# Optimization experiments

Hardware: AMD Instinct MI355X
Metric: run time of the kernel (lower is better)

The kernel has to match this reference:

```python
import jax, jax.numpy as jnp
import numpy as np

N, E, F, H, C = 50000, 800000, 128, 4, 32
SLOPE_ATT = 0.2   # PyG GATConv default negative_slope for attention logits
SLOPE_ACT = 0.01  # torch leaky_relu default between layers


def setup_inputs() -> dict:
    key = jax.random.key(0)
    ks = jax.random.split(key, 12)
    sc = 0.1
    return {
        "x": jax.random.normal(ks[0], (N, F), jnp.float32),
        "edge_index": jax.random.randint(ks[1], (2, E), 0, N, dtype=jnp.int32),
        "W1": jax.random.normal(ks[2], (F, H * C), jnp.float32) * sc,
        "a_src1": jax.random.normal(ks[3], (H, C), jnp.float32) * sc,
        "a_dst1": jax.random.normal(ks[4], (H, C), jnp.float32) * sc,
        "b1": jnp.zeros((H * C,), jnp.float32),
        "W2": jax.random.normal(ks[5], (H * C, H * C), jnp.float32) * sc,
        "a_src2": jax.random.normal(ks[6], (H, C), jnp.float32) * sc,
        "a_dst2": jax.random.normal(ks[7], (H, C), jnp.float32) * sc,
        "b2": jnp.zeros((H * C,), jnp.float32),
        "Wfc": jax.random.normal(ks[8], (H * C, 1), jnp.float32) * sc,
        "bfc": jnp.zeros((1,), jnp.float32),
    }


def gat_layer(x, src, dst, W, a_src, a_dst, bias):
    """PyG-style GATConv: per-head linear, edge attention with leaky_relu,
    segment-softmax over incoming edges of each dst node, scatter-add aggregate."""
    n = x.shape[0]
    h = (x @ W).reshape(n, H, C)                       # [N,H,C]
    att_s = jnp.einsum('nhc,hc->nh', h, a_src)         # per-node src logits
    att_d = jnp.einsum('nhc,hc->nh', h, a_dst)         # per-node dst logits
    e = jax.nn.leaky_relu(att_s[src] + att_d[dst], SLOPE_ATT)   # [Etot,H]
    m = jax.ops.segment_max(e, dst, num_segments=n)    # stable softmax per dst
    e = jnp.exp(e - m[dst])
    z = jax.ops.segment_sum(e, dst, num_segments=n)
    alpha = e / (z[dst] + 1e-16)                       # [Etot,H]
    out = jax.ops.segment_sum(alpha[:, :, None] * h[src], dst, num_segments=n)
    return out.reshape(n, H * C) + bias                # concat heads + bias


def reference(x, edge_index, W1, a_src1, a_dst1, b1, W2, a_src2, a_dst2, b2, Wfc, bfc):
    loops = jnp.arange(N, dtype=edge_index.dtype)      # PyG adds self-loops
    src = jnp.concatenate([edge_index[0], loops])
    dst = jnp.concatenate([edge_index[1], loops])
    h = jax.nn.leaky_relu(gat_layer(x, src, dst, W1, a_src1, a_dst1, b1), SLOPE_ACT)
    h = jax.nn.leaky_relu(gat_layer(h, src, dst, W2, a_src2, a_dst2, b2), SLOPE_ACT)
    return (h @ Wfc + bfc).squeeze(-1)                 # [N]
```

## Files before the change

### kernel.cpp

```cpp
#include <hip/hip_runtime.h>
#include <hip/hip_fp16.h>

#define FD 128

typedef __attribute__((ext_vector_type(8))) short bf16x8;
typedef __attribute__((ext_vector_type(4))) float f32x4;

__device__ __forceinline__ float lrelu(float x, float s){ return x > 0.f ? x : s*x; }

__device__ __forceinline__ unsigned short f2bf(float f){
  unsigned u = __builtin_bit_cast(unsigned, f);
  return (unsigned short)((u + 0x7FFFu + ((u >> 16) & 1u)) >> 16);
}
__device__ __forceinline__ float bf2f(unsigned short h){
  unsigned u = ((unsigned)h) << 16;
  return __builtin_bit_cast(float, u);
}


__global__ __launch_bounds__(256) void count_wprep_kernel(const int* __restrict__ dst,
    int* __restrict__ counts, int E, unsigned rscale, int nchunk, int nbc,
    const float* __restrict__ W1, const float* __restrict__ W2,
    const float* __restrict__ aS1, const float* __restrict__ aD1,
    const float* __restrict__ aS2, const float* __restrict__ aD2,
    unsigned short* __restrict__ WT1, unsigned short* __restrict__ WT2)
{
  int b = blockIdx.x;
  if (b < nbc){
    int xcd = b & 7, chunk = b >> 3;
    int nv = E >> 2;
    for (int v = chunk*256 + threadIdx.x; v < nv; v += nchunk*256){
      int4 d4 = ((const int4*)dst)[v];
      #pragma unroll
      for (int t = 0; t < 4; ++t){
        int d = (&d4.x)[t];
        unsigned r = (unsigned)(((unsigned long long)(unsigned)d * rscale) >> 32);
        if ((int)r == xcd) atomicAdd(&counts[d], 1);
      }
    }
    if (chunk == 0 && threadIdx.x < (E & 3)){
      int i = (E & ~3) + threadIdx.x;
      int d = dst[i];
      unsigned r = (unsigned)(((unsigned long long)(unsigned)d * rscale) >> 32);
      if ((int)r == xcd) atomicAdd(&counts[d], 1);
    }
    return;
  }
  int id = (b - nbc)*256 + threadIdx.x;
  if (id < 32768){
    const float* W = (id < 16384) ? W1 : W2;
    unsigned short* T = (id < 16384) ? WT1 : WT2;
    int idx = id & 16383;
    int k = idx >> 7, c = idx & 127;
    int w = ((c & 7) << 4) | (c >> 3);
    int si = w*128 + (k ^ ((w & 7) << 3));
    float v = W[idx];
    unsigned short h = f2bf(v);
    T[si] = h;
    T[18432 + si] = f2bf(v - bf2f(h));
  } else if (id < 34816){
    int id2 = id - 32768;
    int layer = id2 >> 10;
    int id3 = id2 & 1023;
    int k = id3 >> 3, cc = id3 & 7;
    const float* W  = layer ? W2 : W1;
    const float* av = (cc < 4) ? (layer ? aS2 : aS1) : (layer ? aD2 : aD1);
    unsigned short* T = layer ? WT2 : WT1;
    int h = cc & 3, base = h*32;
    float acc = 0.f;
    #pragma unroll 8
    for (int c = 0; c < 32; ++c) acc += W[k*FD + base + c] * av[base + c];
    int w = 128 + cc;
    int si = w*128 + (k ^ ((w & 7) << 3));
    unsigned short hh = f2bf(acc);
    T[si] = hh;
    T[18432 + si] = f2bf(acc - bf2f(hh));
  } else if (id < 36864){
    int id2 = id - 34816;
    int layer = id2 >> 10;
    int id3 = id2 & 1023;
    int w = 136 + (id3 >> 7), k = id3 & 127;
    unsigned short* T = layer ? WT2 : WT1;
    int si = w*128 + (k ^ ((w & 7) << 3));
    T[si] = 0;
    T[18432 + si] = 0;
  }
}

__global__ __launch_bounds__(512) void scan1_kernel(const int* __restrict__ counts,
    int* __restrict__ offsets, int* __restrict__ blocksum, int n){
  __shared__ int wsum[8];
  int tid = threadIdx.x, lane = tid & 63, wv = tid >> 6;
  int i = blockIdx.x*512 + tid;
  int v = (i < n) ? counts[i] + 1 : 0;
  int incl = v;
  #pragma unroll
  for (int off = 1; off < 64; off <<= 1){
    int t = __shfl_up(incl, off);
    if (lane >= off) incl += t;
  }
  if (lane == 63) wsum[wv] = incl;
  __syncthreads();
  if (wv == 0 && lane < 8){
    int s = wsum[lane];
    #pragma unroll
    for (int off = 1; off < 8; off <<= 1){
      int t = __shfl_up(s, off);
      if (lane >= off) s += t;
    }
    wsum[lane] = s;
  }
  __syncthreads();
  int woff = (wv > 0) ? wsum[wv-1] : 0;
  incl += woff;
  if (i < n) offsets[i] = incl;
  if (tid == 511) blocksum[blockIdx.x] = incl;
}

__global__ __launch_bounds__(512) void scan3_kernel(const int* __restrict__ counts,
    int* __restrict__ offsets, const int* __restrict__ blocksum,
    int* __restrict__ csr, int n, int nsb){
  __shared__ int boff_s;
  int tid = threadIdx.x, b = blockIdx.x;
  if (tid < 64){
    int s = 0;
    for (int j = tid; j < b; j += 64) s += blocksum[j];
    #pragma unroll
    for (int off = 32; off >= 1; off >>= 1) s += __shfl_xor(s, off);
    if (tid == 0) boff_s = s;
  }
  __syncthreads();
  int i = b*512 + tid;
  if (i >= n) return;
  int boff = boff_s;
  int v = counts[i] + 1;
  int gl = offsets[i] + boff;
  offsets[i] = gl - v;
  csr[gl - 1] = i;
  if (i == n - 1) offsets[n] = gl;
}

__global__ __launch_bounds__(256) void fill_part_kernel(const int* __restrict__ ei,
    const int* __restrict__ offsets, int* __restrict__ counts, int* __restrict__ csr,
    int E, unsigned rscale, int nchunk){
  int b = blockIdx.x;
  int xcd = b & 7, chunk = b >> 3;
  int nv = E >> 2;
  for (int v = chunk*256 + threadIdx.x; v < nv; v += nchunk*256){
    int4 s4 = ((const int4*)ei)[v];
    int4 d4 = ((const int4*)(ei + E))[v];
    #pragma unroll
    for (int t = 0; t < 4; ++t){
      int d = (&d4.x)[t];
      unsigned r = (unsigned)(((unsigned long long)(unsigned)d * rscale) >> 32);
      if ((int)r == xcd){
        int c = atomicSub(&counts[d], 1) - 1;
        csr[offsets[d] + c] = (&s4.x)[t];
      }
    }
  }
  if (chunk == 0 && threadIdx.x < (E & 3)){
    int i = (E & ~3) + threadIdx.x;
    int d = ei[E + i];
    unsigned r = (unsigned)(((unsigned long long)(unsigned)d * rscale) >> 32);
    if ((int)r == xcd){
      int c = atomicSub(&counts[d], 1) - 1;
      csr[offsets[d] + c] = ei[i];
    }
  }
}

template<int SPLITIN>
__global__ __launch_bounds__(256) void gemm_mfma_kernel(
    const float* __restrict__ Xf, const unsigned short* __restrict__ X16,
    const unsigned short* __restrict__ WT,
    uint4* __restrict__ H16, float* __restrict__ attS, float* __restrict__ attD, int n)
{
  __shared__ unsigned short smem[36864];
  int tid = threadIdx.x;
  int wv = tid >> 6, lane = tid & 63;
  int g = lane >> 4, r = lane & 15;
  int rbase = blockIdx.x*64 + wv*16;
  int arow = rbase + r; if (arow >= n) arow = n - 1;

  {
    const uint4* src = (const uint4*)WT;
    uint4* dst = (uint4*)smem;
    #pragma unroll
    for (int i = 0; i < 18; ++i) dst[tid + i*256] = src[tid + i*256];
  }

  bf16x8 Ah[4], Al[4];
  if (SPLITIN){
    const uint4* ph = (const uint4*)(X16 + (size_t)arow*FD);
    #pragma unroll
    for (int kc = 0; kc < 4; ++kc){
      uint4 u = ph[kc*4 + g];
      float2 f0 = __half22float2(__builtin_bit_cast(__half2, u.x));
      float2 f1 = __half22float2(__builtin_bit_cast(__half2, u.y));
      float2 f2 = __half22float2(__builtin_bit_cast(__half2, u.z));
      float2 f3 = __half22float2(__builtin_bit_cast(__half2, u.w));
      float xs[8] = {f0.x,f0.y,f1.x,f1.y,f2.x,f2.y,f3.x,f3.y};
      #pragma unroll
      for (int t = 0; t < 8; ++t){
        unsigned short hh = f2bf(xs[t]);
        Ah[kc][t] = (short)hh;
        Al[kc][t] = (short)f2bf(xs[t] - bf2f(hh));
      }
    }
  } else {
    const float4* px = (const float4*)(Xf + (size_t)arow*FD);
    #pragma unroll
    for (int kc = 0; kc < 4; ++kc){
      float4 x0 = px[(kc*4 + g)*2];
      float4 x1 = px[(kc*4 + g)*2 + 1];
      float xs[8] = {x0.x,x0.y,x0.z,x0.w,x1.x,x1.y,x1.z,x1.w};
      #pragma unroll
      for (int t = 0; t < 8; ++t){
        unsigned short hh = f2bf(xs[t]);
        Ah[kc][t] = (short)hh;
        Al[kc][t] = (short)f2bf(xs[t] - bf2f(hh));
      }
    }
  }

  __syncthreads();

  f32x4 acc[9];
  #pragma unroll
  for (int ct = 0; ct < 9; ++ct) acc[ct] = (f32x4){0.f,0.f,0.f,0.f};

  #pragma unroll
  for (int ct = 0; ct < 9; ++ct){
    int wrow = ct*16 + r;
    int sw = (wrow & 7) << 3;
    #pragma unroll
    for (int kc = 0; kc < 4; ++kc){
      int kidx = (kc*32 + g*8) ^ sw;
      bf16x8 Bh = *(const bf16x8*)&smem[wrow*128 + kidx];
      bf16x8 Bl = *(const bf16x8*)&smem[18432 + wrow*128 + kidx];
      acc[ct] = __builtin_amdgcn_mfma_f32_16x16x32_bf16(Ah[kc], Bh, acc[ct], 0, 0, 0);
      acc[ct] = __builtin_amdgcn_mfma_f32_16x16x32_bf16(Ah[kc], Bl, acc[ct], 0, 0, 0);
      acc[ct] = __builtin_amdgcn_mfma_f32_16x16x32_bf16(Al[kc], Bh, acc[ct], 0, 0, 0);
    }
  }

  #pragma unroll
  for (int j = 0; j < 4; ++j){
    int row = rbase + g*4 + j;
    if (row < n){
      __half2 p0 = __float22half2_rn(make_float2(acc[0][j], acc[1][j]));
      __half2 p1 = __float22half2_rn(make_float2(acc[2][j], acc[3][j]));
      __half2 p2 = __float22half2_rn(make_float2(acc[4][j], acc[5][j]));
      __half2 p3 = __float22half2_rn(make_float2(acc[6][j], acc[7][j]));
      uint4 pk;
      pk.x = __builtin_bit_cast(unsigned, p0);
      pk.y = __builtin_bit_cast(unsigned, p1);
      pk.z = __builtin_bit_cast(unsigned, p2);
      pk.w = __builtin_bit_cast(unsigned, p3);
      H16[(size_t)row*16 + r] = pk;
      if (r < 4)      attS[row*4 + r]       = acc[8][j];
      else if (r < 8) attD[row*4 + (r - 4)] = acc[8][j];
    }
  }
}

template<int OUT>
__global__ __launch_bounds__(256) void agg_kernel(
    const uint2* __restrict__ H16, const float* __restrict__ attS, const float* __restrict__ attD,
    const int* __restrict__ csr, const int* __restrict__ offsets,
    const float* __restrict__ bias, const float* __restrict__ wfc, const float* __restrict__ bfc,
    unsigned* __restrict__ o16, float* __restrict__ out, int n)
{
  __shared__ float lds[4][64*5];
  int wid = (int)((blockIdx.x * (size_t)blockDim.x + threadIdx.x) >> 6);
  int lane = threadIdx.x & 63;
  if (wid >= n) return;
  int g = lane >> 4, r = lane & 15;
  int selA = (r >> 3) & 1;
  float* wl = lds[threadIdx.x >> 6];
  int* wli = (int*)wl;

  int start = offsets[wid], end = offsets[wid+1];
  float4 ad4 = ((const float4*)attD)[wid];

  float z0=0.f, z1=0.f, z2=0.f, z3=0.f;
  float acc[8];
  #pragma unroll
  for (int k = 0; k < 8; ++k) acc[k] = 0.f;

  for (int base2 = start; base2 < end; base2 += 64){
    int cnt = end - base2; if (cnt > 64) cnt = 64;
    float p0,p1,p2,p3; int sb = 0;
    if (lane < cnt){
      int s = csr[base2 + lane];
      sb = s << 5;
      float4 as4 = ((const float4*)attS)[s];
      p0 = __expf(lrelu(as4.x + ad4.x, 0.2f));
      p1 = __expf(lrelu(as4.y + ad4.y, 0.2f));
      p2 = __expf(lrelu(as4.z + ad4.z, 0.2f));
      p3 = __expf(lrelu(as4.w + ad4.w, 0.2f));
    } else { p0=p1=p2=p3=0.f; }
    z0+=p0; z1+=p1; z2+=p2; z3+=p3;
    wli[lane*5]  = sb;
    wl[lane*5+1] = p0; wl[lane*5+2] = p1; wl[lane*5+3] = p2; wl[lane*5+4] = p3;
    asm volatile("s_waitcnt lgkmcnt(0)" ::: "memory");
    __builtin_amdgcn_sched_barrier(0);
    for (int jj = g; jj < cnt; jj += 4){
      int sbj  = wli[jj*5];
      float pA = wl[jj*5 + 1 + selA];
      float pB = wl[jj*5 + 3 + selA];
      uint2 u0 = H16[(unsigned)(sbj + r)];
      uint2 u1 = H16[(unsigned)(sbj + 16 + r)];
      float2 a0 = __half22float2(__builtin_bit_cast(__half2, u0.x));
      float2 a1 = __half22float2(__builtin_bit_cast(__half2, u0.y));
      float2 a2 = __half22float2(__builtin_bit_cast(__half2, u1.x));
      float2 a3 = __half22float2(__builtin_bit_cast(__half2, u1.y));
      acc[0] += pA*a0.x; acc[1] += pA*a0.y; acc[2] += pA*a1.x; acc[3] += pA*a1.y;
      acc[4] += pB*a2.x; acc[5] += pB*a2.y; acc[6] += pB*a3.x; acc[7] += pB*a3.y;
    }
    __builtin_amdgcn_sched_barrier(0);
  }

  #pragma unroll
  for (int off = 32; off >= 1; off >>= 1){
    z0+=__shfl_xor(z0,off); z1+=__shfl_xor(z1,off);
    z2+=__shfl_xor(z2,off); z3+=__shfl_xor(z3,off);
  }
  #pragma unroll
  for (int k = 0; k < 8; ++k){
    acc[k] += __shfl_xor(acc[k], 16);
    acc[k] += __shfl_xor(acc[k], 32);
  }
  float o0 = g==0?acc[0]:g==1?acc[2]:g==2?acc[4]:acc[6];
  float o1 = g==0?acc[1]:g==1?acc[3]:g==2?acc[5]:acc[7];
  int ch0 = ((g>>1)<<6) + (r<<2) + ((g&1)<<1);
  float zz = (g < 2) ? ((r<8)? z0 : z1) : ((r<8)? z2 : z3);
  float inv = 1.f / (zz + 1e-16f);
  float2 b2v = ((const float2*)bias)[ch0 >> 1];
  o0 = lrelu(o0*inv + b2v.x, 0.01f);
  o1 = lrelu(o1*inv + b2v.y, 0.01f);
  if (OUT){
    float2 w2v = ((const float2*)wfc)[ch0 >> 1];
    float t = o0*w2v.x + o1*w2v.y;
    #pragma unroll
    for (int off = 32; off >= 1; off >>= 1) t += __shfl_xor(t, off);
    if (lane == 0) out[wid] = t + bfc[0];
  } else {
    __half2 hv = __float22half2_rn(make_float2(o0, o1));
    o16[(size_t)wid*64 + (ch0 >> 1)] = __builtin_bit_cast(unsigned, hv);
  }
}

extern "C" void kernel_launch(void* const* d_in, const int* in_sizes, int n_in,
                              void* d_out, int out_size, void* d_ws, size_t ws_size,
                              hipStream_t stream)
{
  const float* x   = (const float*)d_in[0];
  const int*   ei  = (const int*)d_in[1];
  const float* W1  = (const float*)d_in[2];
  const float* aS1 = (const float*)d_in[3];
  const float* aD1 = (const float*)d_in[4];
  const float* b1  = (const float*)d_in[5];
  const float* W2  = (const float*)d_in[6];
  const float* aS2 = (const float*)d_in[7];
  const float* aD2 = (const float*)d_in[8];
  const float* b2  = (const float*)d_in[9];
  const float* Wfc = (const float*)d_in[10];
  const float* bfc = (const float*)d_in[11];
  float* out = (float*)d_out;

  int n = in_sizes[0] / FD;
  int E = in_sizes[1] / 2;
  int etot = E + n;
  unsigned rscale = (unsigned)(((8ULL << 32) + n - 1) / (unsigned long long)n);

  char* p = (char*)d_ws;
  auto alloc = [&](size_t bytes)->void*{
    void* r = (void*)p;
    p += (bytes + 255) & ~(size_t)255;
    return r;
  };
  int* counts    = (int*)alloc((size_t)n * 4);
  int* offsets   = (int*)alloc((size_t)(n + 1) * 4);
  int* blocksum  = (int*)alloc(1024 * 4);
  int* csr       = (int*)alloc((size_t)etot * 4);
  float* attS1   = (float*)alloc((size_t)n * 4 * 4);
  float* attD1   = (float*)alloc((size_t)n * 4 * 4);
  float* attS2   = (float*)alloc((size_t)n * 4 * 4);
  float* attD2   = (float*)alloc((size_t)n * 4 * 4);
  unsigned short* WT1 = (unsigned short*)alloc(36864*2);
  unsigned short* WT2 = (unsigned short*)alloc(36864*2);
  uint4* H16     = (uint4*)alloc((size_t)n * FD * 2);
  unsigned short* H2 = (unsigned short*)alloc((size_t)n * FD * 2);

  hipMemsetAsync(counts, 0, (size_t)n * 4, stream);

  const int NB_PART = 512;
  int nsb = (n + 511) / 512;
  count_wprep_kernel<<<NB_PART + 144, 256, 0, stream>>>(ei + E, counts, E, rscale,
      NB_PART/8, NB_PART, W1, W2, aS1, aD1, aS2, aD2, WT1, WT2);
  scan1_kernel<<<nsb, 512, 0, stream>>>(counts, offsets, blocksum, n);
  scan3_kernel<<<nsb, 512, 0, stream>>>(counts, offsets, blocksum, csr, n, nsb);
  fill_part_kernel<<<NB_PART, 256, 0, stream>>>(ei, offsets, counts, csr, E, rscale, NB_PART/8);

  int gb = (n + 63) / 64;
  int ab = (int)(((size_t)n * 64 + 255) / 256);

  gemm_mfma_kernel<0><<<gb, 256, 0, stream>>>(x, nullptr, WT1,
                                              H16, attS1, attD1, n);
  agg_kernel<0><<<ab, 256, 0, stream>>>((const uint2*)H16, attS1, attD1, csr, offsets,
                                        b1, nullptr, nullptr, (unsigned*)H2, nullptr, n);
  gemm_mfma_kernel<1><<<gb, 256, 0, stream>>>(nullptr, H2, WT2,
                                              H16, attS2, attD2, n);
  agg_kernel<1><<<ab, 256, 0, stream>>>((const uint2*)H16, attS2, attD2, csr, offsets,
                                        b2, Wfc, bfc, nullptr, out, n);
}
```

Measured before the change: 201.3 us.

## Fuse CSR fill with layer-1 GEMM launch and double rows per GEMM block

The CSR fill kernel and the first-layer GEMM are merged into one launch, with block ranges split between the two tasks so the independent work can run concurrently and one launch boundary disappears. The GEMM body now handles 128 rows per block (two 64-row M tiles per wave group), reusing each LDS-loaded weight fragment across twice as many MFMAs and halving the weight staging per row. The cost is higher register pressure from the doubled accumulators and A fragments, which may lower occupancy. The fused kernel also carries the GEMM's 72KB shared allocation into the fill blocks.

```diff
diff --git a/kernel.cpp b/kernel.cpp
--- a/kernel.cpp
+++ b/kernel.cpp
@@ -140,48 +140,16 @@
   if (i == n - 1) offsets[n] = gl;
 }
 
-__global__ __launch_bounds__(256) void fill_part_kernel(const int* __restrict__ ei,
-    const int* __restrict__ offsets, int* __restrict__ counts, int* __restrict__ csr,
-    int E, unsigned rscale, int nchunk){
-  int b = blockIdx.x;
-  int xcd = b & 7, chunk = b >> 3;
-  int nv = E >> 2;
-  for (int v = chunk*256 + threadIdx.x; v < nv; v += nchunk*256){
-    int4 s4 = ((const int4*)ei)[v];
-    int4 d4 = ((const int4*)(ei + E))[v];
-    #pragma unroll
-    for (int t = 0; t < 4; ++t){
-      int d = (&d4.x)[t];
-      unsigned r = (unsigned)(((unsigned long long)(unsigned)d * rscale) >> 32);
-      if ((int)r == xcd){
-        int c = atomicSub(&counts[d], 1) - 1;
-        csr[offsets[d] + c] = (&s4.x)[t];
-      }
-    }
-  }
-  if (chunk == 0 && threadIdx.x < (E & 3)){
-    int i = (E & ~3) + threadIdx.x;
-    int d = ei[E + i];
-    unsigned r = (unsigned)(((unsigned long long)(unsigned)d * rscale) >> 32);
-    if ((int)r == xcd){
-      int c = atomicSub(&counts[d], 1) - 1;
-      csr[offsets[d] + c] = ei[i];
-    }
-  }
-}
-
 template<int SPLITIN>
-__global__ __launch_bounds__(256) void gemm_mfma_kernel(
+__device__ __forceinline__ void gemm_body(int bid, int tid,
     const float* __restrict__ Xf, const unsigned short* __restrict__ X16,
     const unsigned short* __restrict__ WT,
-    uint4* __restrict__ H16, float* __restrict__ attS, float* __restrict__ attD, int n)
-{
-  __shared__ unsigned short smem[36864];
-  int tid = threadIdx.x;
+    uint4* __restrict__ H16, float* __restrict__ attS, float* __restrict__ attD,
+    int n, unsigned short* smem)
+{
   int wv = tid >> 6, lane = tid & 63;
   int g = lane >> 4, r = lane & 15;
-  int rbase = blockIdx.x*64 + wv*16;
-  int arow = rbase + r; if (arow >= n) arow = n - 1;
+  int rb0 = bid*128 + wv*16;
 
   {
     const uint4* src = (const uint4*)WT;
@@ -190,45 +158,51 @@
     for (int i = 0; i < 18; ++i) dst[tid + i*256] = src[tid + i*256];
   }
 
-  bf16x8 Ah[4], Al[4];
-  if (SPLITIN){
-    const uint4* ph = (const uint4*)(X16 + (size_t)arow*FD);
-    #pragma unroll
-    for (int kc = 0; kc < 4; ++kc){
-      uint4 u = ph[kc*4 + g];
-      float2 f0 = __half22float2(__builtin_bit_cast(__half2, u.x));
-      float2 f1 = __half22float2(__builtin_bit_cast(__half2, u.y));
-      float2 f2 = __half22float2(__builtin_bit_cast(__half2, u.z));
-      float2 f3 = __half22float2(__builtin_bit_cast(__half2, u.w));
-      float xs[8] = {f0.x,f0.y,f1.x,f1.y,f2.x,f2.y,f3.x,f3.y};
+  bf16x8 Ah[2][4], Al[2][4];
+  #pragma unroll
+  for (int m = 0; m < 2; ++m){
+    int arow = rb0 + m*64 + r; if (arow >= n) arow = n - 1;
+    if (SPLITIN){
+      const uint4* ph = (const uint4*)(X16 + (size_t)arow*FD);
       #pragma unroll
-      for (int t = 0; t < 8; ++t){
-        unsigned short hh = f2bf(xs[t]);
-        Ah[kc][t] = (short)hh;
-        Al[kc][t] = (short)f2bf(xs[t] - bf2f(hh));
-      }
-    }
-  } else {
-    const float4* px = (const float4*)(Xf + (size_t)arow*FD);
-    #pragma unroll
-    for (int kc = 0; kc < 4; ++kc){
-      float4 x0 = px[(kc*4 + g)*2];
-      float4 x1 = px[(kc*4 + g)*2 + 1];
-      float xs[8] = {x0.x,x0.y,x0.z,x0.w,x1.x,x1.y,x1.z,x1.w};
+      for (int kc = 0; kc < 4; ++kc){
+        uint4 u = ph[kc*4 + g];
+        float2 f0 = __half22float2(__builtin_bit_cast(__half2, u.x));
+        float2 f1 = __half22float2(__builtin_bit_cast(__half2, u.y));
+        float2 f2 = __half22float2(__builtin_bit_cast(__half2, u.z));
+        float2 f3 = __half22float2(__builtin_bit_cast(__half2, u.w));
+        float xs[8] = {f0.x,f0.y,f1.x,f1.y,f2.x,f2.y,f3.x,f3.y};
+        #pragma unroll
+        for (int t = 0; t < 8; ++t){
+          unsigned short hh = f2bf(xs[t]);
+          Ah[m][kc][t] = (short)hh;
+          Al[m][kc][t] = (short)f2bf(xs[t] - bf2f(hh));
+        }
+      }
+    } else {
+      const float4* px = (const float4*)(Xf + (size_t)arow*FD);
       #pragma unroll
-      for (int t = 0; t < 8; ++t){
-        unsigned short hh = f2bf(xs[t]);
-        Ah[kc][t] = (short)hh;
-        Al[kc][t] = (short)f2bf(xs[t] - bf2f(hh));
+      for (int kc = 0; kc < 4; ++kc){
+        float4 x0 = px[(kc*4 + g)*2];
+        float4 x1 = px[(kc*4 + g)*2 + 1];
+        float xs[8] = {x0.x,x0.y,x0.z,x0.w,x1.x,x1.y,x1.z,x1.w};
+        #pragma unroll
+        for (int t = 0; t < 8; ++t){
+          unsigned short hh = f2bf(xs[t]);
+          Ah[m][kc][t] = (short)hh;
+          Al[m][kc][t] = (short)f2bf(xs[t] - bf2f(hh));
+        }
       }
     }
   }
 
   __syncthreads();
 
-  f32x4 acc[9];
-  #pragma unroll
-  for (int ct = 0; ct < 9; ++ct) acc[ct] = (f32x4){0.f,0.f,0.f,0.f};
+  f32x4 acc[2][9];
+  #pragma unroll
+  for (int m = 0; m < 2; ++m)
+    #pragma unroll
+    for (int ct = 0; ct < 9; ++ct) acc[m][ct] = (f32x4){0.f,0.f,0.f,0.f};
 
   #pragma unroll
   for (int ct = 0; ct < 9; ++ct){
@@ -239,30 +213,82 @@
       int kidx = (kc*32 + g*8) ^ sw;
       bf16x8 Bh = *(const bf16x8*)&smem[wrow*128 + kidx];
       bf16x8 Bl = *(const bf16x8*)&smem[18432 + wrow*128 + kidx];
-      acc[ct] = __builtin_amdgcn_mfma_f32_16x16x32_bf16(Ah[kc], Bh, acc[ct], 0, 0, 0);
-      acc[ct] = __builtin_amdgcn_mfma_f32_16x16x32_bf16(Ah[kc], Bl, acc[ct], 0, 0, 0);
-      acc[ct] = __builtin_amdgcn_mfma_f32_16x16x32_bf16(Al[kc], Bh, acc[ct], 0, 0, 0);
-    }
-  }
-
-  #pragma unroll
-  for (int j = 0; j < 4; ++j){
-    int row = rbase + g*4 + j;
-    if (row < n){
-      __half2 p0 = __float22half2_rn(make_float2(acc[0][j], acc[1][j]));
-      __half2 p1 = __float22half2_rn(make_float2(acc[2][j], acc[3][j]));
-      __half2 p2 = __float22half2_rn(make_float2(acc[4][j], acc[5][j]));
-      __half2 p3 = __float22half2_rn(make_float2(acc[6][j], acc[7][j]));
-      uint4 pk;
-      pk.x = __builtin_bit_cast(unsigned, p0);
-      pk.y = __builtin_bit_cast(unsigned, p1);
-      pk.z = __builtin_bit_cast(unsigned, p2);
-      pk.w = __builtin_bit_cast(unsigned, p3);
-      H16[(size_t)row*16 + r] = pk;
-      if (r < 4)      attS[row*4 + r]       = acc[8][j];
-      else if (r < 8) attD[row*4 + (r - 4)] = acc[8][j];
-    }
-  }
+      #pragma unroll
+      for (int m = 0; m < 2; ++m){
+        acc[m][ct] = __builtin_amdgcn_mfma_f32_16x16x32_bf16(Ah[m][kc], Bh, acc[m][ct], 0, 0, 0);
+        acc[m][ct] = __builtin_amdgcn_mfma_f32_16x16x32_bf16(Ah[m][kc], Bl, acc[m][ct], 0, 0, 0);
+        acc[m][ct] = __builtin_amdgcn_mfma_f32_16x16x32_bf16(Al[m][kc], Bh, acc[m][ct], 0, 0, 0);
+      }
+    }
+  }
+
+  #pragma unroll
+  for (int m = 0; m < 2; ++m){
+    #pragma unroll
+    for (int j = 0; j < 4; ++j){
+      int row = rb0 + m*64 + g*4 + j;
+      if (row < n){
+        __half2 p0 = __float22half2_rn(make_float2(acc[m][0][j], acc[m][1][j]));
+        __half2 p1 = __float22half2_rn(make_float2(acc[m][2][j], acc[m][3][j]));
+        __half2 p2 = __float22half2_rn(make_float2(acc[m][4][j], acc[m][5][j]));
+        __half2 p3 = __float22half2_rn(make_float2(acc[m][6][j], acc[m][7][j]));
+        uint4 pk;
+        pk.x = __builtin_bit_cast(unsigned, p0);
+        pk.y = __builtin_bit_cast(unsigned, p1);
+        pk.z = __builtin_bit_cast(unsigned, p2);
+        pk.w = __builtin_bit_cast(unsigned, p3);
+        H16[(size_t)row*16 + r] = pk;
+        if (r < 4)      attS[row*4 + r]       = acc[m][8][j];
+        else if (r < 8) attD[row*4 + (r - 4)] = acc[m][8][j];
+      }
+    }
+  }
+}
+
+__global__ __launch_bounds__(256) void fill_gemm1_kernel(const int* __restrict__ ei,
+    const int* __restrict__ offsets, int* __restrict__ counts, int* __restrict__ csr,
+    int E, unsigned rscale, int nchunk, int nbf,
+    const float* __restrict__ x, const unsigned short* __restrict__ WT1,
+    uint4* __restrict__ H16, float* __restrict__ attS1, float* __restrict__ attD1, int n)
+{
+  __shared__ unsigned short smem[36864];
+  int b = blockIdx.x;
+  if (b < nbf){
+    int xcd = b & 7, chunk = b >> 3;
+    int nv = E >> 2;
+    for (int v = chunk*256 + threadIdx.x; v < nv; v += nchunk*256){
+      int4 s4 = ((const int4*)ei)[v];
+      int4 d4 = ((const int4*)(ei + E))[v];
+      #pragma unroll
+      for (int t = 0; t < 4; ++t){
+        int d = (&d4.x)[t];
+        unsigned r = (unsigned)(((unsigned long long)(unsigned)d * rscale) >> 32);
+        if ((int)r == xcd){
+          int c = atomicSub(&counts[d], 1) - 1;
+          csr[offsets[d] + c] = (&s4.x)[t];
+        }
+      }
+    }
+    if (chunk == 0 && threadIdx.x < (E & 3)){
+      int i = (E & ~3) + threadIdx.x;
+      int d = ei[E + i];
+      unsigned r = (unsigned)(((unsigned long long)(unsigned)d * rscale) >> 32);
+      if ((int)r == xcd){
+        int c = atomicSub(&counts[d], 1) - 1;
+        csr[offsets[d] + c] = ei[i];
+      }
+    }
+  } else {
+    gemm_body<0>(b - nbf, threadIdx.x, x, nullptr, WT1, H16, attS1, attD1, n, smem);
+  }
+}
+
+__global__ __launch_bounds__(256) void gemm2_kernel(const unsigned short* __restrict__ X16,
+    const unsigned short* __restrict__ WT,
+    uint4* __restrict__ H16, float* __restrict__ attS, float* __restrict__ attD, int n)
+{
+  __shared__ unsigned short smem[36864];
+  gemm_body<1>(blockIdx.x, threadIdx.x, nullptr, X16, WT, H16, attS, attD, n, smem);
 }
 
 template<int OUT>
@@ -398,21 +424,20 @@
 
   const int NB_PART = 512;
   int nsb = (n + 511) / 512;
+  int gb  = (n + 127) / 128;
+
   count_wprep_kernel<<<NB_PART + 144, 256, 0, stream>>>(ei + E, counts, E, rscale,
       NB_PART/8, NB_PART, W1, W2, aS1, aD1, aS2, aD2, WT1, WT2);
   scan1_kernel<<<nsb, 512, 0, stream>>>(counts, offsets, blocksum, n);
   scan3_kernel<<<nsb, 512, 0, stream>>>(counts, offsets, blocksum, csr, n, nsb);
-  fill_part_kernel<<<NB_PART, 256, 0, stream>>>(ei, offsets, counts, csr, E, rscale, NB_PART/8);
-
-  int gb = (n + 63) / 64;
+
+  fill_gemm1_kernel<<<NB_PART + gb, 256, 0, stream>>>(ei, offsets, counts, csr,
+      E, rscale, NB_PART/8, NB_PART, x, WT1, H16, attS1, attD1, n);
+
   int ab = (int)(((size_t)n * 64 + 255) / 256);
-
-  gemm_mfma_kernel<0><<<gb, 256, 0, stream>>>(x, nullptr, WT1,
-                                              H16, attS1, attD1, n);
   agg_kernel<0><<<ab, 256, 0, stream>>>((const uint2*)H16, attS1, attD1, csr, offsets,
                                         b1, nullptr, nullptr, (unsigned*)H2, nullptr, n);
-  gemm_mfma_kernel<1><<<gb, 256, 0, stream>>>(nullptr, H2, WT2,
-                                              H16, attS2, attD2, n);
+  gemm2_kernel<<<gb, 256, 0, stream>>>(H2, WT2, H16, attS2, attD2, n);
   agg_kernel<1><<<ab, 256, 0, stream>>>((const uint2*)H16, attS2, attD2, csr, offsets,
                                         b2, Wfc, bfc, nullptr, out, n);
 }
```

Result: faster. 195.0 us (-3.1%).
